# Performance work log

Measured on AMD Instinct MI355X. Metric: run time of the kernel, lower is better.

## Reference

```python
import jax, jax.numpy as jnp
import numpy as np

N_NODES = 100000
N_EDGES = 1600000
IN_FEAT = 128
HEADS = 4
OUT_FEAT = 16
ALPHA = 0.2  # LeakyReLU negative slope


def setup_inputs() -> dict:
    key = jax.random.key(0)
    k1, k2, k3, k4, k5 = jax.random.split(key, 5)
    x = jax.random.normal(k1, (N_NODES, IN_FEAT), dtype=jnp.float32)
    edge_index = jax.random.randint(k2, (2, N_EDGES), 0, N_NODES, dtype=jnp.int64)
    # xavier_uniform with gain=1.414
    gain = 1.414
    lim_W = gain * np.sqrt(6.0 / (IN_FEAT + HEADS * OUT_FEAT))
    W = jax.random.uniform(k3, (IN_FEAT, HEADS * OUT_FEAT), minval=-lim_W, maxval=lim_W, dtype=jnp.float32)
    lim_a = gain * np.sqrt(6.0 / (HEADS + OUT_FEAT))
    a_src = jax.random.uniform(k4, (HEADS, OUT_FEAT), minval=-lim_a, maxval=lim_a, dtype=jnp.float32)
    a_dst = jax.random.uniform(k5, (HEADS, OUT_FEAT), minval=-lim_a, maxval=lim_a, dtype=jnp.float32)
    return {"x": x, "edge_index": edge_index, "W": W, "a_src": a_src, "a_dst": a_dst}


def reference(x, edge_index, W, a_src, a_dst):
    N = x.shape[0]
    H, F = a_src.shape
    src, dst = edge_index[0], edge_index[1]

    h = (x @ W).reshape(N, H, F)                 # [N, H, F]
    att_src = jnp.sum(h * a_src, axis=-1)        # [N, H]
    att_dst = jnp.sum(h * a_dst, axis=-1)        # [N, H]

    e = jax.nn.leaky_relu(att_src[src] + att_dst[dst], negative_slope=ALPHA)  # [E, H]

    # segment softmax over edges grouped by dst
    e_max = jax.ops.segment_max(e, dst, num_segments=N)   # [N, H]
    e_max = jnp.where(jnp.isfinite(e_max), e_max, 0.0)    # nodes with no in-edges
    ex = jnp.exp(e - e_max[dst])                           # [E, H]
    denom = jax.ops.segment_sum(ex, dst, num_segments=N)  # [N, H]
    alpha = ex / (denom[dst] + 1e-16)                      # [E, H]
    # dropout: inference mode (training=False) -> identity

    messages = h[src] * alpha[:, :, None]                  # [E, H, F]
    out = jax.ops.segment_sum(messages, dst, num_segments=N)  # [N, H, F]

    out = out.reshape(N, H * F)  # concat=True
    out = jax.nn.elu(out)
    return out
```

## Files before the change

kernel.cpp:

```cpp
#include <hip/hip_runtime.h>


#define NEG_SLOPE 0.2f
#define BSHIFT 9
#define BNODES 512
#define CH 2048
#define BCB 512

typedef __bf16 bf16x8 __attribute__((ext_vector_type(8)));
typedef float  f32x4  __attribute__((ext_vector_type(4)));

static __device__ __forceinline__ unsigned f2b(float f) {
    union { float f; unsigned u; } v; v.f = f;
    return (v.u + 0x7fffu + ((v.u >> 16) & 1u)) >> 16;
}
static __device__ __forceinline__ float u2f(unsigned u) {
    union { unsigned u32; float f; } v; v.u32 = u; return v.f;
}

__global__ __launch_bounds__(256) void gemm_att_kernel(
    const float* __restrict__ x,
    const float* __restrict__ W,
    const float* __restrict__ a_src,
    const float* __restrict__ a_dst,
    unsigned short* __restrict__ h_out,
    float* __restrict__ att_s_o,
    float* __restrict__ att_d_o,
    const int* __restrict__ dst,
    int* __restrict__ bucketCount,
    int N, int E, int gemmBlocks)
{
    __shared__ bf16x8 Wswz[20][64];
    __shared__ int c[256];
    int t = threadIdx.x;

    if (blockIdx.x >= gemmBlocks) {
        int bid = blockIdx.x - gemmBlocks;
        c[t] = 0;
        __syncthreads();
        for (int e = bid * 256 + t; e < E; e += BCB * 256)
            atomicAdd(&c[dst[e] >> BSHIFT], 1);
        __syncthreads();
        if (c[t]) atomicAdd(&bucketCount[t], c[t]);
        return;
    }

    for (int i = t; i < 8192; i += 256) {
        int k = i >> 6, n = i & 63;
        __bf16* dp = (__bf16*)&Wswz[((n >> 4) << 2) | (k >> 5)]
                                   [(((k >> 3) & 3) << 4) | (n & 15)];
        dp[k & 7] = (__bf16)W[i];
    }
    for (int i = t; i < 1024; i += 256) {
        int k = i >> 3, c7 = i & 7;
        int hd = c7 & 3;
        const float* aa = (c7 < 4) ? a_src : a_dst;
        float sum = 0.f;
        #pragma unroll
        for (int f = 0; f < 16; ++f)
            sum = fmaf(W[k * 64 + hd * 16 + f], aa[hd * 16 + f], sum);
        __bf16* dp = (__bf16*)&Wswz[16 + (k >> 5)][(((k >> 3) & 3) << 4) | c7];
        dp[k & 7] = (__bf16)sum;
        __bf16* dz = (__bf16*)&Wswz[16 + (k >> 5)][(((k >> 3) & 3) << 4) | (8 + c7)];
        dz[k & 7] = (__bf16)0.f;
    }
    __syncthreads();

    int wave = t >> 6;
    int lane = t & 63;
    int col = lane & 15, quad = lane >> 4;
    int node_base = (blockIdx.x * 4 + wave) * 16;
    int arow = min(node_base + col, N - 1);
    const float* xp = x + arow * 128;

    bf16x8 af[4];
    #pragma unroll
    for (int tt = 0; tt < 4; ++tt) {
        float4 xa = *(const float4*)(xp + tt * 32 + quad * 8);
        float4 xb = *(const float4*)(xp + tt * 32 + quad * 8 + 4);
        bf16x8 f;
        f[0] = (__bf16)xa.x; f[1] = (__bf16)xa.y;
        f[2] = (__bf16)xa.z; f[3] = (__bf16)xa.w;
        f[4] = (__bf16)xb.x; f[5] = (__bf16)xb.y;
        f[6] = (__bf16)xb.z; f[7] = (__bf16)xb.w;
        af[tt] = f;
    }

    f32x4 acc[4], accA;
    #pragma unroll
    for (int cb = 0; cb < 4; ++cb) {
        acc[cb] = (f32x4){0.f, 0.f, 0.f, 0.f};
        #pragma unroll
        for (int tt = 0; tt < 4; ++tt)
            acc[cb] = __builtin_amdgcn_mfma_f32_16x16x32_bf16(
                af[tt], Wswz[(cb << 2) | tt][lane], acc[cb], 0, 0, 0);
    }
    accA = (f32x4){0.f, 0.f, 0.f, 0.f};
    #pragma unroll
    for (int tt = 0; tt < 4; ++tt)
        accA = __builtin_amdgcn_mfma_f32_16x16x32_bf16(
            af[tt], Wswz[16 + tt][lane], accA, 0, 0, 0);

    #pragma unroll
    for (int cb = 0; cb < 4; ++cb) {
        #pragma unroll
        for (int r = 0; r < 4; ++r) {
            int node = node_base + quad * 4 + r;
            if (node < N)
                h_out[node * 64 + cb * 16 + col] = (unsigned short)f2b(acc[cb][r]);
        }
    }
    if (col < 8) {
        #pragma unroll
        for (int r = 0; r < 4; ++r) {
            int node = node_base + quad * 4 + r;
            if (node < N) {
                if (col < 4) att_s_o[(node << 2) | col] = accA[r];
                else         att_d_o[(node << 2) | (col - 4)] = accA[r];
            }
        }
    }
}

__global__ __launch_bounds__(256) void bscatter_kernel(
    const int* __restrict__ src, const int* __restrict__ dst,
    const int* __restrict__ bucketCount,
    int* __restrict__ bucketCursor, int* __restrict__ pairs, int nb, int E)
{
    __shared__ int cnt[256], lo[256], gpos[256], cur[256], sm[256], gbc[256];
    __shared__ int2 staged[CH];
    int t = threadIdx.x;
    int base = blockIdx.x * CH;
    int nloc = min(CH, E - base);

    cnt[t] = 0;
    gbc[t] = (t < nb) ? bucketCount[t] : 0;
    __syncthreads();
    for (int i = t; i < nloc; i += 256)
        atomicAdd(&cnt[dst[base + i] >> BSHIFT], 1);
    __syncthreads();

    int v = cnt[t];
    sm[t] = v;
    __syncthreads();
    #pragma unroll
    for (int off = 1; off < 256; off <<= 1) {
        int u = (t >= off) ? sm[t - off] : 0;
        __syncthreads();
        sm[t] += u;
        __syncthreads();
    }
    lo[t] = sm[t] - v;
    cur[t] = lo[t];
    __syncthreads();

    int g = gbc[t];
    sm[t] = g;
    __syncthreads();
    #pragma unroll
    for (int off = 1; off < 256; off <<= 1) {
        int u = (t >= off) ? sm[t - off] : 0;
        __syncthreads();
        sm[t] += u;
        __syncthreads();
    }
    gpos[t] = (v > 0) ? (sm[t] - g) + atomicAdd(&bucketCursor[t], v) : 0;
    __syncthreads();

    for (int i = t; i < nloc; i += 256) {
        int d = dst[base + i];
        int s = src[base + i];
        int b = d >> BSHIFT;
        int k = atomicAdd(&cur[b], 1);
        staged[k] = make_int2((s << BSHIFT) | (d & (BNODES - 1)), b);
    }
    __syncthreads();

    for (int i = t; i < nloc; i += 256) {
        int2 p = staged[i];
        pairs[gpos[p.y] + (i - lo[p.y])] = p.x;
    }
}

__global__ __launch_bounds__(1024) void csrfill_kernel(
    const int* __restrict__ pairs, const int* __restrict__ bucketCount,
    int* __restrict__ rowstart, int* __restrict__ elsrc, int nb, int N, int E)
{
    __shared__ int hist[512], cur[512], sm[512], gbc[256], gsm[256];
    int b = blockIdx.x, t = threadIdx.x;
    int node_lo = b << BSHIFT;
    int nn = min(BNODES, N - node_lo);

    if (t < 256) { gbc[t] = (t < nb) ? bucketCount[t] : 0; gsm[t] = gbc[t]; }
    if (t < 512) hist[t] = 0;
    __syncthreads();
    #pragma unroll
    for (int off = 1; off < 256; off <<= 1) {
        int u = (t >= off && t < 256) ? gsm[t - off] : 0;
        __syncthreads();
        if (t < 256) gsm[t] += u;
        __syncthreads();
    }
    int ebase = gsm[b] - gbc[b];
    int ecnt = gbc[b];

    for (int i = t; i < ecnt; i += 1024)
        atomicAdd(&hist[pairs[ebase + i] & (BNODES - 1)], 1);
    __syncthreads();

    int v = (t < 512) ? hist[t] : 0;
    if (t < 512) sm[t] = v;
    __syncthreads();
    #pragma unroll
    for (int off = 1; off < 512; off <<= 1) {
        int u = (t >= off && t < 512) ? sm[t - off] : 0;
        __syncthreads();
        if (t < 512) sm[t] += u;
        __syncthreads();
    }
    if (t < 512) {
        int excl = sm[t] - v;
        cur[t] = excl;
        if (t < nn) rowstart[node_lo + t] = ebase + excl;
    }
    if (b == gridDim.x - 1 && t == 0) rowstart[N] = E;
    __syncthreads();

    for (int i = t; i < ecnt; i += 1024) {
        int p = pairs[ebase + i];
        int k = atomicAdd(&cur[p & (BNODES - 1)], 1);
        elsrc[ebase + k] = p >> BSHIFT;
    }
}

__global__ __launch_bounds__(256) void agg_kernel(
    const int* __restrict__ elsrc,
    const int* __restrict__ rowstart,
    const float* __restrict__ att_s,
    const float* __restrict__ att_d,
    const unsigned short* __restrict__ hmat,
    float* __restrict__ out,
    int N)
{
    int node = blockIdx.x * 4 + (threadIdx.x >> 6);
    if (node >= N) return;
    int lane = threadIdx.x & 63;
    int q = lane & 7;
    int eslot = lane >> 3;
    int h = q >> 1;

    int beg = rowstart[node];
    int deg = rowstart[node + 1] - beg;
    float ad = att_d[(node << 2) | h];

    float a0 = 0.f, a1 = 0.f, a2 = 0.f, a3 = 0.f;
    float a4 = 0.f, a5 = 0.f, a6 = 0.f, a7 = 0.f, l = 0.f;

    for (int base = 0; base < deg; base += 8) {
        int e = base + eslot;
        int idx = beg + min(e, deg - 1);
        int s = elsrc[idx];
        float av = att_s[(s << 2) | h] + ad;
        av = fmaxf(av, NEG_SLOPE * av);
        float w = (e < deg) ? __expf(av) : 0.f;
        l += w;
        uint4 hp = *(const uint4*)(hmat + (s << 6) + (q << 3));
        a0 = fmaf(w, u2f(hp.x << 16), a0);
        a1 = fmaf(w, u2f(hp.x & 0xffff0000u), a1);
        a2 = fmaf(w, u2f(hp.y << 16), a2);
        a3 = fmaf(w, u2f(hp.y & 0xffff0000u), a3);
        a4 = fmaf(w, u2f(hp.z << 16), a4);
        a5 = fmaf(w, u2f(hp.z & 0xffff0000u), a5);
        a6 = fmaf(w, u2f(hp.w << 16), a6);
        a7 = fmaf(w, u2f(hp.w & 0xffff0000u), a7);
    }

    #pragma unroll
    for (int m = 8; m <= 32; m <<= 1) {
        a0 += __shfl_xor(a0, m, 64);
        a1 += __shfl_xor(a1, m, 64);
        a2 += __shfl_xor(a2, m, 64);
        a3 += __shfl_xor(a3, m, 64);
        a4 += __shfl_xor(a4, m, 64);
        a5 += __shfl_xor(a5, m, 64);
        a6 += __shfl_xor(a6, m, 64);
        a7 += __shfl_xor(a7, m, 64);
        l  += __shfl_xor(l,  m, 64);
    }

    if (eslot == 0) {
        float rl = 1.0f / (l + 1e-16f);
        float4 v0, v1;
        v0.x = a0 * rl; v0.x = (v0.x > 0.f) ? v0.x : (__expf(v0.x) - 1.f);
        v0.y = a1 * rl; v0.y = (v0.y > 0.f) ? v0.y : (__expf(v0.y) - 1.f);
        v0.z = a2 * rl; v0.z = (v0.z > 0.f) ? v0.z : (__expf(v0.z) - 1.f);
        v0.w = a3 * rl; v0.w = (v0.w > 0.f) ? v0.w : (__expf(v0.w) - 1.f);
        v1.x = a4 * rl; v1.x = (v1.x > 0.f) ? v1.x : (__expf(v1.x) - 1.f);
        v1.y = a5 * rl; v1.y = (v1.y > 0.f) ? v1.y : (__expf(v1.y) - 1.f);
        v1.z = a6 * rl; v1.z = (v1.z > 0.f) ? v1.z : (__expf(v1.z) - 1.f);
        v1.w = a7 * rl; v1.w = (v1.w > 0.f) ? v1.w : (__expf(v1.w) - 1.f);
        float* op = out + (node << 6) + (q << 3);
        *(float4*)op = v0;
        *(float4*)(op + 4) = v1;
    }
}

extern "C" void kernel_launch(void* const* d_in, const int* in_sizes, int n_in,
                              void* d_out, int out_size, void* d_ws, size_t ws_size,
                              hipStream_t stream) {
    const float* x     = (const float*)d_in[0];
    const int*   ei    = (const int*)d_in[1];
    const float* W     = (const float*)d_in[2];
    const float* a_src = (const float*)d_in[3];
    const float* a_dst = (const float*)d_in[4];

    int N = in_sizes[0] / 128;
    int E = in_sizes[1] / 2;
    const int* src = ei;
    const int* dst = ei + E;
    int nb = (N + BNODES - 1) / BNODES;

    char* ws = (char*)d_ws;
    size_t off = 0;
    unsigned short* hmat = (unsigned short*)(ws + off); off += (size_t)N * 64 * 2;
    float* att_s = (float*)(ws + off);  off += (size_t)N * 4 * 4;
    float* att_d = (float*)(ws + off);  off += (size_t)N * 4 * 4;
    int* rowstart = (int*)(ws + off);   off += (size_t)(N + 1) * 4;
    int* elsrc    = (int*)(ws + off);   off += (size_t)E * 4;
    int* pairs    = (int*)(ws + off);   off += (size_t)E * 4;
    int* bucketCount  = (int*)(ws + off); off += 256 * 4;
    int* bucketCursor = (int*)(ws + off); off += 256 * 4;

    hipMemsetAsync(bucketCount, 0, 512 * 4, stream);

    int gemmBlocks = (N + 63) / 64;
    gemm_att_kernel<<<gemmBlocks + BCB, 256, 0, stream>>>(
        x, W, a_src, a_dst, hmat, att_s, att_d, dst, bucketCount,
        N, E, gemmBlocks);

    int blocksS = (E + CH - 1) / CH;
    bscatter_kernel<<<blocksS, 256, 0, stream>>>(src, dst, bucketCount,
                                                 bucketCursor, pairs, nb, E);

    csrfill_kernel<<<nb, 1024, 0, stream>>>(pairs, bucketCount,
                                            rowstart, elsrc, nb, N, E);

    int blocksA = (N + 3) / 4;
    agg_kernel<<<blocksA, 256, 0, stream>>>(elsrc, rowstart, att_s, att_d,
                                            hmat, (float*)d_out, N);
}
```

Before: 228.4 us.

## Fuse CSR fill and aggregation into per-bucket shared-memory atomic accumulation

Removes the csrfill kernel and the per-node aggregation kernel. One 1024-thread block per 512-node destination bucket now reads the bucket's edge pairs directly and accumulates weighted features and softmax denominators in a padded LDS buffer (about 140 KB) using float atomics, then applies normalization and ELU. This drops the second sort pass and the rowstart/elsrc traffic. In exchange it adds heavy LDS atomic contention, runs only one block per CU across about 196 blocks, and makes float summation order nondeterministic.

```diff
diff --git a/kernel.cpp b/kernel.cpp
--- a/kernel.cpp
+++ b/kernel.cpp
@@ -6,6 +6,10 @@
 #define BNODES 512
 #define CH 2048
 #define BCB 512
+
+#define ACC_STRIDE 513
+#define ACC_WORDS (64 * ACC_STRIDE)
+#define SM_WORDS (ACC_WORDS + BNODES * 4)
 
 typedef __bf16 bf16x8 __attribute__((ext_vector_type(8)));
 typedef float  f32x4  __attribute__((ext_vector_type(4)));
@@ -182,126 +186,71 @@
     }
 }
 
-__global__ __launch_bounds__(1024) void csrfill_kernel(
-    const int* __restrict__ pairs, const int* __restrict__ bucketCount,
-    int* __restrict__ rowstart, int* __restrict__ elsrc, int nb, int N, int E)
-{
-    __shared__ int hist[512], cur[512], sm[512], gbc[256], gsm[256];
-    int b = blockIdx.x, t = threadIdx.x;
-    int node_lo = b << BSHIFT;
-    int nn = min(BNODES, N - node_lo);
-
-    if (t < 256) { gbc[t] = (t < nb) ? bucketCount[t] : 0; gsm[t] = gbc[t]; }
-    if (t < 512) hist[t] = 0;
-    __syncthreads();
-    #pragma unroll
-    for (int off = 1; off < 256; off <<= 1) {
-        int u = (t >= off && t < 256) ? gsm[t - off] : 0;
-        __syncthreads();
-        if (t < 256) gsm[t] += u;
-        __syncthreads();
-    }
-    int ebase = gsm[b] - gbc[b];
-    int ecnt = gbc[b];
-
-    for (int i = t; i < ecnt; i += 1024)
-        atomicAdd(&hist[pairs[ebase + i] & (BNODES - 1)], 1);
-    __syncthreads();
-
-    int v = (t < 512) ? hist[t] : 0;
-    if (t < 512) sm[t] = v;
-    __syncthreads();
-    #pragma unroll
-    for (int off = 1; off < 512; off <<= 1) {
-        int u = (t >= off && t < 512) ? sm[t - off] : 0;
-        __syncthreads();
-        if (t < 512) sm[t] += u;
-        __syncthreads();
-    }
-    if (t < 512) {
-        int excl = sm[t] - v;
-        cur[t] = excl;
-        if (t < nn) rowstart[node_lo + t] = ebase + excl;
-    }
-    if (b == gridDim.x - 1 && t == 0) rowstart[N] = E;
-    __syncthreads();
-
-    for (int i = t; i < ecnt; i += 1024) {
-        int p = pairs[ebase + i];
-        int k = atomicAdd(&cur[p & (BNODES - 1)], 1);
-        elsrc[ebase + k] = p >> BSHIFT;
-    }
-}
-
-__global__ __launch_bounds__(256) void agg_kernel(
-    const int* __restrict__ elsrc,
-    const int* __restrict__ rowstart,
+__global__ __launch_bounds__(1024) void bucket_agg_kernel(
+    const int* __restrict__ pairs,
+    const int* __restrict__ bucketCount,
     const float* __restrict__ att_s,
     const float* __restrict__ att_d,
     const unsigned short* __restrict__ hmat,
     float* __restrict__ out,
-    int N)
+    int nb, int N)
 {
-    int node = blockIdx.x * 4 + (threadIdx.x >> 6);
-    if (node >= N) return;
-    int lane = threadIdx.x & 63;
-    int q = lane & 7;
-    int eslot = lane >> 3;
+    extern __shared__ float smf[];
+    float* acc  = smf;
+    float* lsum = smf + ACC_WORDS;
+    __shared__ int gbc[256], gsm[256];
+
+    int b = blockIdx.x, t = threadIdx.x;
+    int node_lo = b << BSHIFT;
+    int nn = min(BNODES, N - node_lo);
+
+    float4 z4 = make_float4(0.f, 0.f, 0.f, 0.f);
+    for (int i = t; i < SM_WORDS / 4; i += 1024)
+        ((float4*)smf)[i] = z4;
+
+    if (t < 256) { int g = (t < nb) ? bucketCount[t] : 0; gbc[t] = g; gsm[t] = g; }
+    __syncthreads();
+    #pragma unroll
+    for (int off = 1; off < 256; off <<= 1) {
+        int u = (t >= off && t < 256) ? gsm[t - off] : 0;
+        __syncthreads();
+        if (t < 256) gsm[t] += u;
+        __syncthreads();
+    }
+    int ebase = gsm[b] - gbc[b];
+    int ecnt  = gbc[b];
+
+    int q = t & 7;
     int h = q >> 1;
-
-    int beg = rowstart[node];
-    int deg = rowstart[node + 1] - beg;
-    float ad = att_d[(node << 2) | h];
-
-    float a0 = 0.f, a1 = 0.f, a2 = 0.f, a3 = 0.f;
-    float a4 = 0.f, a5 = 0.f, a6 = 0.f, a7 = 0.f, l = 0.f;
-
-    for (int base = 0; base < deg; base += 8) {
-        int e = base + eslot;
-        int idx = beg + min(e, deg - 1);
-        int s = elsrc[idx];
-        float av = att_s[(s << 2) | h] + ad;
+    float* ap0 = acc + (q << 3) * ACC_STRIDE;
+
+    for (int i = t >> 3; i < ecnt; i += 128) {
+        int p = pairs[ebase + i];
+        int s = p >> BSHIFT;
+        int dloc = p & (BNODES - 1);
+        float av = att_s[(s << 2) | h] + att_d[((node_lo + dloc) << 2) | h];
         av = fmaxf(av, NEG_SLOPE * av);
-        float w = (e < deg) ? __expf(av) : 0.f;
-        l += w;
+        float w = __expf(av);
+        if (!(q & 1)) atomicAdd(&lsum[(dloc << 2) | h], w);
         uint4 hp = *(const uint4*)(hmat + (s << 6) + (q << 3));
-        a0 = fmaf(w, u2f(hp.x << 16), a0);
-        a1 = fmaf(w, u2f(hp.x & 0xffff0000u), a1);
-        a2 = fmaf(w, u2f(hp.y << 16), a2);
-        a3 = fmaf(w, u2f(hp.y & 0xffff0000u), a3);
-        a4 = fmaf(w, u2f(hp.z << 16), a4);
-        a5 = fmaf(w, u2f(hp.z & 0xffff0000u), a5);
-        a6 = fmaf(w, u2f(hp.w << 16), a6);
-        a7 = fmaf(w, u2f(hp.w & 0xffff0000u), a7);
-    }
-
-    #pragma unroll
-    for (int m = 8; m <= 32; m <<= 1) {
-        a0 += __shfl_xor(a0, m, 64);
-        a1 += __shfl_xor(a1, m, 64);
-        a2 += __shfl_xor(a2, m, 64);
-        a3 += __shfl_xor(a3, m, 64);
-        a4 += __shfl_xor(a4, m, 64);
-        a5 += __shfl_xor(a5, m, 64);
-        a6 += __shfl_xor(a6, m, 64);
-        a7 += __shfl_xor(a7, m, 64);
-        l  += __shfl_xor(l,  m, 64);
-    }
-
-    if (eslot == 0) {
-        float rl = 1.0f / (l + 1e-16f);
-        float4 v0, v1;
-        v0.x = a0 * rl; v0.x = (v0.x > 0.f) ? v0.x : (__expf(v0.x) - 1.f);
-        v0.y = a1 * rl; v0.y = (v0.y > 0.f) ? v0.y : (__expf(v0.y) - 1.f);
-        v0.z = a2 * rl; v0.z = (v0.z > 0.f) ? v0.z : (__expf(v0.z) - 1.f);
-        v0.w = a3 * rl; v0.w = (v0.w > 0.f) ? v0.w : (__expf(v0.w) - 1.f);
-        v1.x = a4 * rl; v1.x = (v1.x > 0.f) ? v1.x : (__expf(v1.x) - 1.f);
-        v1.y = a5 * rl; v1.y = (v1.y > 0.f) ? v1.y : (__expf(v1.y) - 1.f);
-        v1.z = a6 * rl; v1.z = (v1.z > 0.f) ? v1.z : (__expf(v1.z) - 1.f);
-        v1.w = a7 * rl; v1.w = (v1.w > 0.f) ? v1.w : (__expf(v1.w) - 1.f);
-        float* op = out + (node << 6) + (q << 3);
-        *(float4*)op = v0;
-        *(float4*)(op + 4) = v1;
+        float* ap = ap0 + dloc;
+        atomicAdd(ap + 0 * ACC_STRIDE, w * u2f(hp.x << 16));
+        atomicAdd(ap + 1 * ACC_STRIDE, w * u2f(hp.x & 0xffff0000u));
+        atomicAdd(ap + 2 * ACC_STRIDE, w * u2f(hp.y << 16));
+        atomicAdd(ap + 3 * ACC_STRIDE, w * u2f(hp.y & 0xffff0000u));
+        atomicAdd(ap + 4 * ACC_STRIDE, w * u2f(hp.z << 16));
+        atomicAdd(ap + 5 * ACC_STRIDE, w * u2f(hp.z & 0xffff0000u));
+        atomicAdd(ap + 6 * ACC_STRIDE, w * u2f(hp.w << 16));
+        atomicAdd(ap + 7 * ACC_STRIDE, w * u2f(hp.w & 0xffff0000u));
+    }
+    __syncthreads();
+
+    for (int i = t; i < (nn << 6); i += 1024) {
+        int node = i >> 6, f = i & 63;
+        float rl = 1.f / (lsum[(node << 2) | (f >> 4)] + 1e-16f);
+        float v = acc[f * ACC_STRIDE + node] * rl;
+        v = (v > 0.f) ? v : (__expf(v) - 1.f);
+        out[((node_lo + node) << 6) | f] = v;
     }
 }
 
@@ -325,13 +274,15 @@
     unsigned short* hmat = (unsigned short*)(ws + off); off += (size_t)N * 64 * 2;
     float* att_s = (float*)(ws + off);  off += (size_t)N * 4 * 4;
     float* att_d = (float*)(ws + off);  off += (size_t)N * 4 * 4;
-    int* rowstart = (int*)(ws + off);   off += (size_t)(N + 1) * 4;
-    int* elsrc    = (int*)(ws + off);   off += (size_t)E * 4;
     int* pairs    = (int*)(ws + off);   off += (size_t)E * 4;
     int* bucketCount  = (int*)(ws + off); off += 256 * 4;
     int* bucketCursor = (int*)(ws + off); off += 256 * 4;
 
     hipMemsetAsync(bucketCount, 0, 512 * 4, stream);
+
+    hipFuncSetAttribute((const void*)bucket_agg_kernel,
+                        hipFuncAttributeMaxDynamicSharedMemorySize,
+                        SM_WORDS * 4);
 
     int gemmBlocks = (N + 63) / 64;
     gemm_att_kernel<<<gemmBlocks + BCB, 256, 0, stream>>>(
@@ -342,10 +293,6 @@
     bscatter_kernel<<<blocksS, 256, 0, stream>>>(src, dst, bucketCount,
                                                  bucketCursor, pairs, nb, E);
 
-    csrfill_kernel<<<nb, 1024, 0, stream>>>(pairs, bucketCount,
-                                            rowstart, elsrc, nb, N, E);
-
-    int blocksA = (N + 3) / 4;
-    agg_kernel<<<blocksA, 256, 0, stream>>>(elsrc, rowstart, att_s, att_d,
-                                            hmat, (float*)d_out, N);
-}
+    bucket_agg_kernel<<<nb, 1024, SM_WORDS * 4, stream>>>(
+        pairs, bucketCount, att_s, att_d, hmat, (float*)d_out, nb, N);
+}
```

Result: slower. 886.6 us (+288.2%).
